# Kernel optimization log

Measured on AMD Instinct MI355X. Metric: run time of the kernel, lower is better.

## Reference

```python
import jax, jax.numpy as jnp
import numpy as np

N, D, E, H, TOPK = 16384, 1024, 8, 4096, 2


def setup_inputs() -> dict:
    key = jax.random.key(0)
    ks = jax.random.split(key, 7)
    s_in = 1.0 / np.sqrt(D)
    s_h = 1.0 / np.sqrt(H)
    return {
        "x": jax.random.normal(ks[0], (N, D), jnp.float32),
        "Wg": jax.random.uniform(ks[1], (D, E), jnp.float32, -s_in, s_in),
        "bg": jnp.zeros((E,), jnp.float32),
        "W1": jax.random.uniform(ks[2], (E, D, H), jnp.float32, -s_in, s_in),
        "b1": jax.random.uniform(ks[3], (E, H), jnp.float32, -s_in, s_in),
        "W2": jax.random.uniform(ks[4], (E, H, D), jnp.float32, -s_h, s_h),
        "b2": jax.random.uniform(ks[5], (E, D), jnp.float32, -s_h, s_h),
    }


def _moe_forward(x, Wg, bg, W1, b1, W2, b2):
    # Gate: softmax over experts, top-k, renormalize (standard TopKGate)
    logits = x @ Wg + bg                       # (N, E)
    probs = jax.nn.softmax(logits, axis=-1)
    gates, idxs = jax.lax.top_k(probs, TOPK)   # (N, K)
    gates = gates / jnp.sum(gates, axis=-1, keepdims=True)

    # combine weight per token per expert: cw[n,e] = sum_k gates[n,k]*[idxs[n,k]==e]
    onehot = jax.nn.one_hot(idxs, E, dtype=x.dtype)        # (N, K, E)
    cw = jnp.einsum("nk,nke->ne", gates, onehot)           # (N, E)

    # per-expert 2-layer MLP, gated combine (loop over small fixed expert set)
    out = jnp.zeros_like(x)
    for e in range(E):
        h = jax.nn.relu(x @ W1[e] + b1[e])     # (N, H)
        y = h @ W2[e] + b2[e]                  # (N, D)
        out = out + cw[:, e:e + 1] * y

    # aux loss: for each expert with >=1 routed token, add mean(gates[:,0])^2
    counts = jnp.sum(onehot, axis=(0, 1))                  # (E,)
    active = (counts > 0).astype(x.dtype)                  # (E,)
    m = jnp.mean(gates[:, 0])
    aux_loss = jnp.sum(active) * m * m
    return out, aux_loss


def reference(x, Wg, bg, W1, b1, W2, b2):
    return _moe_forward(x, Wg, bg, W1, b1, W2, b2)
```

## Files before the change

kernel.cpp:

```cpp
#include <hip/hip_runtime.h>
#include <stdint.h>

typedef unsigned short u16;
typedef __bf16 bf16x8 __attribute__((ext_vector_type(8)));
typedef float f32x4 __attribute__((ext_vector_type(4)));

#define N_TOK 16384
#define DIM   1024
#define NEXP  8
#define HID   4096
#define MTILES 264
#define PADROWS 33792

__device__ __forceinline__ u16 f2bf(float f) {
  uint32_t u = __builtin_bit_cast(uint32_t, f);
  u += 0x7fffu + ((u >> 16) & 1u);
  return (u16)(u >> 16);
}

__device__ __forceinline__ void gload16(const void* g, void* l) {
  __builtin_amdgcn_global_load_lds(
      (const __attribute__((address_space(1))) uint32_t*)g,
      (__attribute__((address_space(3))) uint32_t*)l, 16, 0, 0);
}


__global__ void k_zero(int* counts) {
  if (threadIdx.x < NEXP) counts[threadIdx.x] = 0;
}

__global__ void k_tcast(const float* __restrict__ src, u16* __restrict__ dst,
                        int R, int C) {
  __shared__ float tile[32][33];
  int nc = C >> 5, nr = R >> 5;
  int t = blockIdx.x;
  int cb = t % nc; t /= nc;
  int rb = t % nr; int ee = t / nr;
  const float* s0 = src + ((size_t)ee * R + (size_t)rb * 32) * C + cb * 32;
  int tx = threadIdx.x & 31, ty = threadIdx.x >> 5;
#pragma unroll
  for (int i = 0; i < 4; ++i)
    tile[ty + i * 8][tx] = s0[(size_t)(ty + i * 8) * C + tx];
  __syncthreads();
  u16* d0 = dst + ((size_t)ee * C + (size_t)cb * 32) * R + rb * 32;
#pragma unroll
  for (int i = 0; i < 4; ++i)
    d0[(size_t)(ty + i * 8) * R + tx] = f2bf(tile[tx][ty + i * 8]);
}


__global__ __launch_bounds__(256) void k_gate(
    const float* __restrict__ x, const float* __restrict__ Wg,
    const float* __restrict__ bg, u16* __restrict__ xb,
    int* __restrict__ tok_e, float* __restrict__ tok_g,
    float* __restrict__ blocksums) {
  __shared__ float wg_s[NEXP * DIM];
  __shared__ float s4[4];
  for (int i = threadIdx.x; i < NEXP * DIM; i += 256) {
    int k = i >> 3, e = i & 7;
    wg_s[e * DIM + k] = Wg[i];
  }
  __syncthreads();
  int lane = threadIdx.x & 63, wv = threadIdx.x >> 6;
  int n = blockIdx.x * 4 + wv;
  const float4* xr4 = (const float4*)(x + (size_t)n * DIM);
  float4 xv[4];
#pragma unroll
  for (int i = 0; i < 4; ++i) xv[i] = xr4[lane + 64 * i];
  ushort4* xo4 = (ushort4*)(xb + (size_t)n * DIM);
#pragma unroll
  for (int i = 0; i < 4; ++i) {
    ushort4 p;
    p.x = f2bf(xv[i].x); p.y = f2bf(xv[i].y);
    p.z = f2bf(xv[i].z); p.w = f2bf(xv[i].w);
    xo4[lane + 64 * i] = p;
  }
  float acc[8];
#pragma unroll
  for (int e = 0; e < 8; ++e) {
    const float4* w4 = (const float4*)(wg_s + e * DIM);
    float a = 0.f;
#pragma unroll
    for (int i = 0; i < 4; ++i) {
      float4 wv4 = w4[lane + 64 * i];
      a += xv[i].x * wv4.x + xv[i].y * wv4.y + xv[i].z * wv4.z +
           xv[i].w * wv4.w;
    }
    acc[e] = a;
  }
#pragma unroll
  for (int e = 0; e < 8; ++e)
#pragma unroll
    for (int off = 32; off > 0; off >>= 1)
      acc[e] += __shfl_xor(acc[e], off);

  if (lane == 0) {
    float l0 = -1e30f, l1 = -1e30f; int e0 = 0, e1 = 0;
#pragma unroll
    for (int e = 0; e < 8; ++e) {
      float v = acc[e] + bg[e];
      if (v > l0) { l1 = l0; e1 = e0; l0 = v; e0 = e; }
      else if (v > l1) { l1 = v; e1 = e; }
    }
    float g0 = 1.f / (1.f + expf(l1 - l0));
    float g1 = 1.f - g0;
    tok_e[2 * n] = e0; tok_e[2 * n + 1] = e1;
    tok_g[2 * n] = g0; tok_g[2 * n + 1] = g1;
    s4[wv] = g0;
  }
  __syncthreads();
  if (threadIdx.x == 0) blocksums[blockIdx.x] = s4[0] + s4[1] + s4[2] + s4[3];
}


__global__ __launch_bounds__(256) void k_hist(const int* __restrict__ tok_e,
                                              int* __restrict__ counts) {
  __shared__ int lcnt[8];
  if (threadIdx.x < 8) lcnt[threadIdx.x] = 0;
  __syncthreads();
  int base4 = (blockIdx.x * 256 + threadIdx.x) * 2;
  const int4* t4 = (const int4*)tok_e;
  int4 a = t4[base4], b = t4[base4 + 1];
  int v[8] = {a.x, a.y, a.z, a.w, b.x, b.y, b.z, b.w};
  int c[8];
#pragma unroll
  for (int ee = 0; ee < 8; ++ee) {
    int s = 0;
#pragma unroll
    for (int i = 0; i < 8; ++i) s += (v[i] == ee);
    c[ee] = s;
  }
  int lane = threadIdx.x & 63;
#pragma unroll
  for (int ee = 0; ee < 8; ++ee) {
    int s = c[ee];
#pragma unroll
    for (int off = 32; off > 0; off >>= 1) s += __shfl_xor(s, off);
    if (lane == 0 && s) atomicAdd(&lcnt[ee], s);
  }
  __syncthreads();
  if (threadIdx.x < 8 && lcnt[threadIdx.x])
    atomicAdd(&counts[threadIdx.x], lcnt[threadIdx.x]);
}


__global__ __launch_bounds__(256) void k_setup(
    const int* __restrict__ counts, const float* __restrict__ blocksums,
    int* __restrict__ padded_off, int* __restrict__ cursor,
    int* __restrict__ row2tok, float* __restrict__ row2gate,
    float* __restrict__ aux_out) {
  __shared__ float red[256];
  __shared__ int off_s[9];
  float s = 0.f;
  for (int i = threadIdx.x; i < 4096; i += 256) s += blocksums[i];
  red[threadIdx.x] = s;
  __syncthreads();
  for (int st = 128; st > 0; st >>= 1) {
    if (threadIdx.x < st) red[threadIdx.x] += red[threadIdx.x + st];
    __syncthreads();
  }
  if (threadIdx.x == 0) {
    int off = 0, nact = 0;
    for (int e = 0; e < 8; ++e) {
      off_s[e] = off;
      int c = counts[e];
      if (c > 0) nact++;
      off += ((c + 127) >> 7) << 7;
      cursor[e] = 0;
    }
    off_s[8] = off;
    for (int e = 0; e <= 8; ++e) padded_off[e] = off_s[e];
    float m = red[0] / (float)N_TOK;
    *aux_out = (float)nact * m * m;
  }
  __syncthreads();
  for (int idx = threadIdx.x; idx < NEXP * 128; idx += 256) {
    int e = idx >> 7, i = idx & 127;
    int slot = off_s[e] + counts[e] + i;
    if (slot < off_s[e + 1]) { row2tok[slot] = 0; row2gate[slot] = 0.f; }
  }
}


__global__ __launch_bounds__(256) void k_scatter(
    const int* __restrict__ tok_e, const float* __restrict__ tok_g,
    const int* __restrict__ padded_off, int* __restrict__ cursor,
    int* __restrict__ row2tok, float* __restrict__ row2gate) {
  __shared__ int lcnt[8], lbase[8];
  if (threadIdx.x < 8) lcnt[threadIdx.x] = 0;
  __syncthreads();
  int n = blockIdx.x * 256 + threadIdx.x;
  int e0 = tok_e[2 * n], e1 = tok_e[2 * n + 1];
  int p0 = atomicAdd(&lcnt[e0], 1);
  int p1 = atomicAdd(&lcnt[e1], 1);
  __syncthreads();
  if (threadIdx.x < 8 && lcnt[threadIdx.x])
    lbase[threadIdx.x] = atomicAdd(&cursor[threadIdx.x], lcnt[threadIdx.x]);
  __syncthreads();
  int s0 = padded_off[e0] + lbase[e0] + p0;
  int s1 = padded_off[e1] + lbase[e1] + p1;
  row2tok[s0] = n; row2gate[s0] = tok_g[2 * n];
  row2tok[s1] = n; row2gate[s1] = tok_g[2 * n + 1];
}


template <int KDIM, int MODE>
__global__ __launch_bounds__(256, 3) void k_gemm(
    const u16* __restrict__ Asrc, const u16* __restrict__ Wt,
    const float* __restrict__ bias, const int* __restrict__ row2tok,
    const float* __restrict__ row2gate, const int* __restrict__ padded_off,
    void* __restrict__ Out) {
  __shared__ u16 Abuf[3][4096];
  __shared__ u16 Bbuf[3][4096];
  constexpr int NDIM = MODE ? DIM : HID;
  int row0 = blockIdx.y * 128;
  if (row0 >= padded_off[8]) return;
  int e = 0;
  while (row0 >= padded_off[e + 1]) ++e;
  int n0 = blockIdx.x * 128;
  int tid = threadIdx.x, lane = tid & 63, wv = tid >> 6;
  int wm = wv >> 1, wn = wv & 1;
  int fr = lane & 15, fq = lane >> 4;
  int ra0 = tid >> 2, ra1 = 64 + (tid >> 2);
  int ca = (tid & 3) * 8;
  const u16 *asrc0, *asrc1;
  if (MODE == 0) {
    asrc0 = Asrc + (size_t)row2tok[row0 + ra0] * KDIM + ca;
    asrc1 = Asrc + (size_t)row2tok[row0 + ra1] * KDIM + ca;
  } else {
    asrc0 = Asrc + (size_t)(row0 + ra0) * KDIM + ca;
    asrc1 = Asrc + (size_t)(row0 + ra1) * KDIM + ca;
  }
  const u16* bb = Wt + (size_t)e * (HID * DIM);
  const u16* bsrc0 = bb + (size_t)(n0 + ra0) * KDIM + ca;
  const u16* bsrc1 = bb + (size_t)(n0 + ra1) * KDIM + ca;
  int lo = wv * 512;

  f32x4 acc[4][4];
#pragma unroll
  for (int i = 0; i < 4; ++i)
#pragma unroll
    for (int j = 0; j < 4; ++j) acc[i][j] = (f32x4){0.f, 0.f, 0.f, 0.f};
  bf16x8 av[4], bv[4];

#define STG(b, kt)                                 \
  do {                                             \
    int ko = (kt) * 32;                            \
    gload16(asrc0 + ko, &Abuf[b][lo]);             \
    gload16(asrc1 + ko, &Abuf[b][2048 + lo]);      \
    gload16(bsrc0 + ko, &Bbuf[b][lo]);             \
    gload16(bsrc1 + ko, &Bbuf[b][2048 + lo]);      \
  } while (0)

#define CMP(b)                                                                 \
  do {                                                                         \
    _Pragma("unroll") for (int fm = 0; fm < 4; ++fm)                           \
        av[fm] = *(const bf16x8*)&Abuf[b][(wm * 64 + fm * 16 + fr) * 32 + fq * 8]; \
    _Pragma("unroll") for (int fn = 0; fn < 4; ++fn)                           \
        bv[fn] = *(const bf16x8*)&Bbuf[b][(wn * 64 + fn * 16 + fr) * 32 + fq * 8]; \
    _Pragma("unroll") for (int fm = 0; fm < 4; ++fm)                           \
        _Pragma("unroll") for (int fn = 0; fn < 4; ++fn)                       \
            acc[fm][fn] = __builtin_amdgcn_mfma_f32_16x16x32_bf16(             \
                av[fm], bv[fn], acc[fm][fn], 0, 0, 0);                         \
  } while (0)

  constexpr int NK = KDIM / 32;
  STG(0, 0);
  STG(1, 1);
  int rb = 0;
  for (int kt = 0; kt < NK - 2; ++kt) {
    int sb = rb + 2; if (sb >= 3) sb -= 3;
    STG(sb, kt + 2);
    asm volatile("s_waitcnt vmcnt(8)" ::: "memory");
    __builtin_amdgcn_s_barrier();
    CMP(rb);
    __builtin_amdgcn_s_barrier();
    if (++rb == 3) rb = 0;
  }
  asm volatile("s_waitcnt vmcnt(4)" ::: "memory");
  __builtin_amdgcn_s_barrier();
  CMP(rb);
  if (++rb == 3) rb = 0;
  __builtin_amdgcn_s_barrier();
  asm volatile("s_waitcnt vmcnt(0)" ::: "memory");
  __builtin_amdgcn_s_barrier();
  CMP(rb);
#undef STG
#undef CMP

  float bv4[4];
#pragma unroll
  for (int fn = 0; fn < 4; ++fn)
    bv4[fn] = bias[e * NDIM + n0 + wn * 64 + fn * 16 + fr];

  if (MODE == 0) {
    u16* hp = (u16*)Out;
#pragma unroll
    for (int fm = 0; fm < 4; ++fm) {
#pragma unroll
      for (int j = 0; j < 4; ++j) {
        int grow = row0 + wm * 64 + fm * 16 + fq * 4 + j;
        u16* hr = hp + (size_t)grow * HID + n0 + wn * 64 + fr;
#pragma unroll
        for (int fn = 0; fn < 4; ++fn) {
          float v = acc[fm][fn][j] + bv4[fn];
          hr[fn * 16] = f2bf(v > 0.f ? v : 0.f);
        }
      }
    }
  } else {
    float* op = (float*)Out;
#pragma unroll
    for (int fm = 0; fm < 4; ++fm) {
#pragma unroll
      for (int j = 0; j < 4; ++j) {
        int grow = row0 + wm * 64 + fm * 16 + fq * 4 + j;
        int tok = row2tok[grow];
        float g = row2gate[grow];
        float* orow = op + (size_t)tok * DIM + n0 + wn * 64 + fr;
#pragma unroll
        for (int fn = 0; fn < 4; ++fn)
          atomicAdd(orow + fn * 16, g * (acc[fm][fn][j] + bv4[fn]));
      }
    }
  }
}


extern "C" void kernel_launch(void* const* d_in, const int* in_sizes, int n_in,
                              void* d_out, int out_size, void* d_ws,
                              size_t ws_size, hipStream_t stream) {
  const float* x  = (const float*)d_in[0];
  const float* Wg = (const float*)d_in[1];
  const float* bg = (const float*)d_in[2];
  const float* W1 = (const float*)d_in[3];
  const float* b1 = (const float*)d_in[4];
  const float* W2 = (const float*)d_in[5];
  const float* b2 = (const float*)d_in[6];
  float* out = (float*)d_out;

  char* w = (char*)d_ws;
  u16* xb          = (u16*)(w);
  u16* w1t         = (u16*)(w + 33554432);
  u16* w2t         = (u16*)(w + 100663296);
  u16* h           = (u16*)(w + 167772160);
  int* tok_e       = (int*)(w + 444596224);
  float* tok_g     = (float*)(w + 444727296);
  int* counts      = (int*)(w + 444858368);
  int* cursor      = (int*)(w + 444858624);
  int* padded_off  = (int*)(w + 444858880);
  int* row2tok     = (int*)(w + 444859136);
  float* row2gate  = (float*)(w + 444994304);
  float* blocksums = (float*)(w + 445129472);

  k_zero<<<1, 64, 0, stream>>>(counts);
  k_gate<<<4096, 256, 0, stream>>>(x, Wg, bg, xb, tok_e, tok_g, blocksums);
  k_hist<<<16, 256, 0, stream>>>(tok_e, counts);
  hipMemsetAsync(d_out, 0, (size_t)N_TOK * DIM * sizeof(float), stream);
  k_setup<<<1, 256, 0, stream>>>(counts, blocksums, padded_off, cursor, row2tok,
                                 row2gate, out + (size_t)N_TOK * DIM);
  k_scatter<<<64, 256, 0, stream>>>(tok_e, tok_g, padded_off, cursor, row2tok,
                                    row2gate);
  k_tcast<<<32768, 256, 0, stream>>>(W1, w1t, DIM, HID);
  k_tcast<<<32768, 256, 0, stream>>>(W2, w2t, HID, DIM);
  k_gemm<DIM, 0><<<dim3(HID / 128, MTILES), 256, 0, stream>>>(
      xb, w1t, b1, row2tok, row2gate, padded_off, h);
  k_gemm<HID, 1><<<dim3(DIM / 128, MTILES), 256, 0, stream>>>(
      h, w2t, b2, row2tok, row2gate, padded_off, out);
}
```

Measured before the change: 966.7 us.

## Replace atomic scatter-add with bf16 expert output buffer and gather combine kernel

The second GEMM now writes bf16 per-slot outputs to a staging buffer that reuses the xb workspace, instead of doing fp32 atomicAdds into the output. A new combine kernel gathers each token's two slot rows and applies the gate weights. This also removes the output memset and the row2gate array, and k_scatter writes slot indices back into tok_e. The GEMM barrier sequence is also changed to inline-asm s_barrier with an explicit lgkmcnt wait, dropping one barrier in the tail. The cost is an extra kernel launch and a bf16 rounding of expert outputs before the combine.

Result: faster. 887.6 us (-8.2%).

```diff
diff --git a/kernel.cpp b/kernel.cpp
--- a/kernel.cpp
+++ b/kernel.cpp
@@ -16,6 +16,11 @@
   uint32_t u = __builtin_bit_cast(uint32_t, f);
   u += 0x7fffu + ((u >> 16) & 1u);
   return (u16)(u >> 16);
+}
+
+__device__ __forceinline__ float bf2f(u16 v) {
+  uint32_t u = (uint32_t)v << 16;
+  return __builtin_bit_cast(float, u);
 }
 
 __device__ __forceinline__ void gload16(const void* g, void* l) {
@@ -147,8 +152,7 @@
 __global__ __launch_bounds__(256) void k_setup(
     const int* __restrict__ counts, const float* __restrict__ blocksums,
     int* __restrict__ padded_off, int* __restrict__ cursor,
-    int* __restrict__ row2tok, float* __restrict__ row2gate,
-    float* __restrict__ aux_out) {
+    int* __restrict__ row2tok, float* __restrict__ aux_out) {
   __shared__ float red[256];
   __shared__ int off_s[9];
   float s = 0.f;
@@ -177,15 +181,14 @@
   for (int idx = threadIdx.x; idx < NEXP * 128; idx += 256) {
     int e = idx >> 7, i = idx & 127;
     int slot = off_s[e] + counts[e] + i;
-    if (slot < off_s[e + 1]) { row2tok[slot] = 0; row2gate[slot] = 0.f; }
+    if (slot < off_s[e + 1]) row2tok[slot] = 0;
   }
 }
 
 
 __global__ __launch_bounds__(256) void k_scatter(
-    const int* __restrict__ tok_e, const float* __restrict__ tok_g,
-    const int* __restrict__ padded_off, int* __restrict__ cursor,
-    int* __restrict__ row2tok, float* __restrict__ row2gate) {
+    int* __restrict__ tok_e, const int* __restrict__ padded_off,
+    int* __restrict__ cursor, int* __restrict__ row2tok) {
   __shared__ int lcnt[8], lbase[8];
   if (threadIdx.x < 8) lcnt[threadIdx.x] = 0;
   __syncthreads();
@@ -199,8 +202,10 @@
   __syncthreads();
   int s0 = padded_off[e0] + lbase[e0] + p0;
   int s1 = padded_off[e1] + lbase[e1] + p1;
-  row2tok[s0] = n; row2gate[s0] = tok_g[2 * n];
-  row2tok[s1] = n; row2gate[s1] = tok_g[2 * n + 1];
+  row2tok[s0] = n;
+  row2tok[s1] = n;
+  tok_e[2 * n] = s0;
+  tok_e[2 * n + 1] = s1;
 }
 
 
@@ -208,8 +213,7 @@
 __global__ __launch_bounds__(256, 3) void k_gemm(
     const u16* __restrict__ Asrc, const u16* __restrict__ Wt,
     const float* __restrict__ bias, const int* __restrict__ row2tok,
-    const float* __restrict__ row2gate, const int* __restrict__ padded_off,
-    void* __restrict__ Out) {
+    const int* __restrict__ padded_off, u16* __restrict__ Out) {
   __shared__ u16 Abuf[3][4096];
   __shared__ u16 Bbuf[3][4096];
   constexpr int NDIM = MODE ? DIM : HID;
@@ -272,18 +276,18 @@
     int sb = rb + 2; if (sb >= 3) sb -= 3;
     STG(sb, kt + 2);
     asm volatile("s_waitcnt vmcnt(8)" ::: "memory");
-    __builtin_amdgcn_s_barrier();
+    asm volatile("s_barrier" ::: "memory");
     CMP(rb);
-    __builtin_amdgcn_s_barrier();
+    asm volatile("s_waitcnt lgkmcnt(0)" ::: "memory");
+    asm volatile("s_barrier" ::: "memory");
     if (++rb == 3) rb = 0;
   }
   asm volatile("s_waitcnt vmcnt(4)" ::: "memory");
-  __builtin_amdgcn_s_barrier();
+  asm volatile("s_barrier" ::: "memory");
   CMP(rb);
   if (++rb == 3) rb = 0;
-  __builtin_amdgcn_s_barrier();
   asm volatile("s_waitcnt vmcnt(0)" ::: "memory");
-  __builtin_amdgcn_s_barrier();
+  asm volatile("s_barrier" ::: "memory");
   CMP(rb);
 #undef STG
 #undef CMP
@@ -293,37 +297,38 @@
   for (int fn = 0; fn < 4; ++fn)
     bv4[fn] = bias[e * NDIM + n0 + wn * 64 + fn * 16 + fr];
 
-  if (MODE == 0) {
-    u16* hp = (u16*)Out;
-#pragma unroll
-    for (int fm = 0; fm < 4; ++fm) {
-#pragma unroll
-      for (int j = 0; j < 4; ++j) {
-        int grow = row0 + wm * 64 + fm * 16 + fq * 4 + j;
-        u16* hr = hp + (size_t)grow * HID + n0 + wn * 64 + fr;
-#pragma unroll
-        for (int fn = 0; fn < 4; ++fn) {
-          float v = acc[fm][fn][j] + bv4[fn];
-          hr[fn * 16] = f2bf(v > 0.f ? v : 0.f);
-        }
+#pragma unroll
+  for (int fm = 0; fm < 4; ++fm) {
+#pragma unroll
+    for (int j = 0; j < 4; ++j) {
+      int grow = row0 + wm * 64 + fm * 16 + fq * 4 + j;
+      u16* orow = Out + (size_t)grow * NDIM + n0 + wn * 64 + fr;
+#pragma unroll
+      for (int fn = 0; fn < 4; ++fn) {
+        float v = acc[fm][fn][j] + bv4[fn];
+        if (MODE == 0) v = v > 0.f ? v : 0.f;
+        orow[fn * 16] = f2bf(v);
       }
     }
-  } else {
-    float* op = (float*)Out;
-#pragma unroll
-    for (int fm = 0; fm < 4; ++fm) {
-#pragma unroll
-      for (int j = 0; j < 4; ++j) {
-        int grow = row0 + wm * 64 + fm * 16 + fq * 4 + j;
-        int tok = row2tok[grow];
-        float g = row2gate[grow];
-        float* orow = op + (size_t)tok * DIM + n0 + wn * 64 + fr;
-#pragma unroll
-        for (int fn = 0; fn < 4; ++fn)
-          atomicAdd(orow + fn * 16, g * (acc[fm][fn][j] + bv4[fn]));
-      }
-    }
-  }
+  }
+}
+
+
+__global__ __launch_bounds__(256) void k_combine(
+    const u16* __restrict__ y, const int* __restrict__ slots,
+    const float* __restrict__ tok_g, float* __restrict__ out) {
+  int n = blockIdx.x;
+  int s0 = slots[2 * n], s1 = slots[2 * n + 1];
+  float g0 = tok_g[2 * n], g1 = tok_g[2 * n + 1];
+  int d = threadIdx.x * 4;
+  ushort4 a = *(const ushort4*)(y + (size_t)s0 * DIM + d);
+  ushort4 b = *(const ushort4*)(y + (size_t)s1 * DIM + d);
+  float4 o;
+  o.x = g0 * bf2f(a.x) + g1 * bf2f(b.x);
+  o.y = g0 * bf2f(a.y) + g1 * bf2f(b.y);
+  o.z = g0 * bf2f(a.z) + g1 * bf2f(b.z);
+  o.w = g0 * bf2f(a.w) + g1 * bf2f(b.w);
+  *(float4*)(out + (size_t)n * DIM + d) = o;
 }
 
 
@@ -341,6 +346,7 @@
 
   char* w = (char*)d_ws;
   u16* xb          = (u16*)(w);
+  u16* y           = (u16*)(w);
   u16* w1t         = (u16*)(w + 33554432);
   u16* w2t         = (u16*)(w + 100663296);
   u16* h           = (u16*)(w + 167772160);
@@ -350,21 +356,19 @@
   int* cursor      = (int*)(w + 444858624);
   int* padded_off  = (int*)(w + 444858880);
   int* row2tok     = (int*)(w + 444859136);
-  float* row2gate  = (float*)(w + 444994304);
   float* blocksums = (float*)(w + 445129472);
 
   k_zero<<<1, 64, 0, stream>>>(counts);
   k_gate<<<4096, 256, 0, stream>>>(x, Wg, bg, xb, tok_e, tok_g, blocksums);
   k_hist<<<16, 256, 0, stream>>>(tok_e, counts);
-  hipMemsetAsync(d_out, 0, (size_t)N_TOK * DIM * sizeof(float), stream);
   k_setup<<<1, 256, 0, stream>>>(counts, blocksums, padded_off, cursor, row2tok,
-                                 row2gate, out + (size_t)N_TOK * DIM);
-  k_scatter<<<64, 256, 0, stream>>>(tok_e, tok_g, padded_off, cursor, row2tok,
-                                    row2gate);
+                                 out + (size_t)N_TOK * DIM);
+  k_scatter<<<64, 256, 0, stream>>>(tok_e, padded_off, cursor, row2tok);
   k_tcast<<<32768, 256, 0, stream>>>(W1, w1t, DIM, HID);
   k_tcast<<<32768, 256, 0, stream>>>(W2, w2t, HID, DIM);
   k_gemm<DIM, 0><<<dim3(HID / 128, MTILES), 256, 0, stream>>>(
-      xb, w1t, b1, row2tok, row2gate, padded_off, h);
+      xb, w1t, b1, row2tok, padded_off, h);
   k_gemm<HID, 1><<<dim3(DIM / 128, MTILES), 256, 0, stream>>>(
-      h, w2t, b2, row2tok, row2gate, padded_off, out);
-}
+      h, w2t, b2, row2tok, padded_off, y);
+  k_combine<<<N_TOK, 256, 0, stream>>>(y, tok_e, tok_g, out);
+}
```
